# Kernel tuning notes

Measured on AMD Instinct MI355X. Metric: run time of the kernel, lower is better.

Reference implementation:

```python
import jax, jax.numpy as jnp
import numpy as np

A, C, V, G = 100000, 230, 800, 60          # athletes, countries, events, games
H, HEADS, DH = 128, 4, 32                   # hidden, gat heads, per-head dim (H = HEADS*DH)
E_AC, E_AE, E_AG, E_EG = 100000, 500000, 300000, 2000
NEG_SLOPE = 0.2


def _seg_mean(msg, idx, n):
    s = jax.ops.segment_sum(msg, idx, num_segments=n)
    cnt = jax.ops.segment_sum(jnp.ones((idx.shape[0], 1), msg.dtype), idx, num_segments=n)
    return s / jnp.maximum(cnt, 1.0)


def _sage(xs, xd, ei, Wl, bl, Wr):
    # PyG SAGEConv(mean): lin_l(mean_neighbors) + lin_r(x_dst); bias lives in lin_l
    agg = _seg_mean(xs[ei[0]], ei[1], xd.shape[0])
    return agg @ Wl + bl + xd @ Wr


def _gatv2(xs, xd, ei, Wl, bl, Wr, br, att, bias):
    # PyG GATv2Conv, concat=True, add_self_loops=False, eval mode (no dropout)
    n = xd.shape[0]
    xl = (xs @ Wl + bl).reshape(-1, HEADS, DH)   # [Ns,H,d]
    xr = (xd @ Wr + br).reshape(-1, HEADS, DH)   # [Nd,H,d]
    src, dst = ei[0], ei[1]
    e = jax.nn.leaky_relu(xl[src] + xr[dst], NEG_SLOPE)      # [E,H,d]
    logit = jnp.einsum('ehd,hd->eh', e, att)                 # [E,H]
    m = jax.ops.segment_max(logit, dst, num_segments=n)
    m = jnp.where(jnp.isneginf(m), 0.0, m)                   # empty dst segments
    ex = jnp.exp(logit - m[dst])
    den = jax.ops.segment_sum(ex, dst, num_segments=n)
    alpha = ex / (den[dst] + 1e-16)
    out = jax.ops.segment_sum(xl[src] * alpha[:, :, None], dst, num_segments=n)
    return out.reshape(n, HEADS * DH) + bias


def _mlp(x, W1, b1, W2, b2):
    return jax.nn.relu(x @ W1 + b1) @ W2 + b2


def _forward(x_athlete, x_country, x_event, x_games,
             eAW1, eAb1, eAW2, eAb2, eCW1, eCb1, eCW2, eCb2,
             eEW1, eEb1, eEW2, eEb2, eGW1, eGb1, eGW2, eGb2,
             sage_Wl, sage_bl, sage_Wr,
             gat_Wl, gat_bl, gat_Wr, gat_br, gat_att, gat_bias,
             ei_ac, ei_ae, ei_ag, ei_eg):
    x = {
        'athlete': _mlp(x_athlete, eAW1, eAb1, eAW2, eAb2),
        'country': _mlp(x_country, eCW1, eCb1, eCW2, eCb2),
        'event':   _mlp(x_event,   eEW1, eEb1, eEW2, eEb2),
        'games':   _mlp(x_games,   eGW1, eGb1, eGW2, eGb2),
    }
    rev = lambda ei: ei[::-1]
    etypes = [
        ('athlete', 'country', ei_ac), ('country', 'athlete', rev(ei_ac)),
        ('athlete', 'event',   ei_ae), ('event',   'athlete', rev(ei_ae)),
        ('athlete', 'games',   ei_ag), ('games',   'athlete', rev(ei_ag)),
        ('event',   'games',   ei_eg), ('games',   'event',   rev(ei_eg)),
    ]
    # layer 1: hetero SAGEConv, HeteroConv aggr='mean' over edge types per dst
    outs = {t: [] for t in x}
    for k, (s, d, ei) in enumerate(etypes):
        outs[d].append(_sage(x[s], x[d], ei, sage_Wl[k], sage_bl[k], sage_Wr[k]))
    x = {t: jax.nn.relu(sum(o) / len(o)) for t, o in outs.items()}
    # layer 2 (final): hetero GATv2Conv, mean over edge types per dst
    outs = {t: [] for t in x}
    for k, (s, d, ei) in enumerate(etypes):
        outs[d].append(_gatv2(x[s], x[d], ei, gat_Wl[k], gat_bl[k], gat_Wr[k],
                              gat_br[k], gat_att[k], gat_bias[k]))
    x = {t: sum(o) / len(o) for t, o in outs.items()}
    return jnp.concatenate([x['athlete'], x['country'], x['event'], x['games']], axis=0)


def setup_inputs() -> dict:
    key = jax.random.key(0)
    ks = iter(jax.random.split(key, 80))
    def nrm(shape, scale=1.0):
        return jax.random.normal(next(ks), shape, jnp.float32) * scale
    def lin(fi, fo):
        return nrm((fi, fo), 1.0 / np.sqrt(fi))
    def edges(ns, nd, E):
        s = jax.random.randint(next(ks), (E,), 0, ns)
        d = jax.random.randint(next(ks), (E,), 0, nd)
        return jnp.stack([s, d]).astype(jnp.int32)
    sc = 1.0 / np.sqrt(H)
    return {
        'x_athlete': nrm((A, 7)), 'x_country': nrm((C, 3)),
        'x_event': nrm((V, 384)), 'x_games': nrm((G, 2)),
        'ei_ac': edges(A, C, E_AC), 'ei_ae': edges(A, V, E_AE),
        'ei_ag': edges(A, G, E_AG), 'ei_eg': edges(V, G, E_EG),
        'eAW1': lin(7, H),   'eAb1': jnp.zeros((H,)), 'eAW2': lin(H, H), 'eAb2': jnp.zeros((H,)),
        'eCW1': lin(3, H),   'eCb1': jnp.zeros((H,)), 'eCW2': lin(H, H), 'eCb2': jnp.zeros((H,)),
        'eEW1': lin(384, H), 'eEb1': jnp.zeros((H,)), 'eEW2': lin(H, H), 'eEb2': jnp.zeros((H,)),
        'eGW1': lin(2, H),   'eGb1': jnp.zeros((H,)), 'eGW2': lin(H, H), 'eGb2': jnp.zeros((H,)),
        'sage_Wl': nrm((8, H, H), sc), 'sage_bl': jnp.zeros((8, H)), 'sage_Wr': nrm((8, H, H), sc),
        'gat_Wl': nrm((8, H, H), sc), 'gat_bl': jnp.zeros((8, H)),
        'gat_Wr': nrm((8, H, H), sc), 'gat_br': jnp.zeros((8, H)),
        'gat_att': nrm((8, HEADS, DH), 1.0 / np.sqrt(DH)), 'gat_bias': jnp.zeros((8, H)),
    }


def reference(x_athlete, x_country, x_event, x_games,
              eAW1, eAb1, eAW2, eAb2, eCW1, eCb1, eCW2, eCb2,
              eEW1, eEb1, eEW2, eEb2, eGW1, eGb1, eGW2, eGb2,
              sage_Wl, sage_bl, sage_Wr,
              gat_Wl, gat_bl, gat_Wr, gat_br, gat_att, gat_bias,
              ei_ac, ei_ae, ei_ag, ei_eg):
    return _forward(x_athlete, x_country, x_event, x_games,
                    eAW1, eAb1, eAW2, eAb2, eCW1, eCb1, eCW2, eCb2,
                    eEW1, eEb1, eEW2, eEb2, eGW1, eGb1, eGW2, eGb2,
                    sage_Wl, sage_bl, sage_Wr,
                    gat_Wl, gat_bl, gat_Wr, gat_br, gat_att, gat_bias,
                    ei_ac, ei_ae, ei_ag, ei_eg)
```

## Files before the change

### kernel.cpp

```cpp
#include <hip/hip_runtime.h>
#include <hip/hip_bf16.h>

#define A_N 100000
#define C_N 230
#define V_N 800
#define G_N 60

#define FLAG_RELU 2

#define SCAN_N   302080
#define SCAN_NB  295
#define E_TOTAL  1804000

#define PCHUNK 16

typedef __attribute__((ext_vector_type(8))) short short8;
typedef __attribute__((ext_vector_type(4))) float f32x4;

__device__ __forceinline__ float bf16dec(unsigned short u){
  return __uint_as_float(((unsigned)u) << 16);
}
__device__ __forceinline__ unsigned short f2b(float v){
  union { __hip_bfloat16 h; unsigned short u; } c;
  c.h = __float2bfloat16(v);
  return c.u;
}
__device__ __forceinline__ float4 ldb4(const unsigned short* p){
  uint2 v = *(const uint2*)p;
  float4 r;
  r.x = __uint_as_float(v.x << 16);
  r.y = __uint_as_float(v.x & 0xffff0000u);
  r.z = __uint_as_float(v.y << 16);
  r.w = __uint_as_float(v.y & 0xffff0000u);
  return r;
}
static inline int imin(int a, int b){ return a < b ? a : b; }

__global__ void detect_dtype(const unsigned short* __restrict__ p, int* __restrict__ flag){
  __shared__ int bad;
  if (threadIdx.x == 0) bad = 0;
  __syncthreads();
  for (int i = threadIdx.x; i < 2048; i += blockDim.x){
    float v = fabsf(bf16dec(p[i]));
    if (!(v <= 1e6f)) atomicOr(&bad, 1);
  }
  __syncthreads();
  if (threadIdx.x == 0) *flag = bad;
}

struct ConvTab { const void* src[29]; int dstoff[29]; int cum[30]; };

__global__ void convert_all(ConvTab tab, float* __restrict__ wsf,
                            const int* __restrict__ flagp, int total){
  const int f = *flagp;
  for (int idx = blockIdx.x*blockDim.x + threadIdx.x; idx < total;
       idx += gridDim.x*blockDim.x){
    int t = 0;
    while (idx >= tab.cum[t+1]) ++t;
    int l = idx - tab.cum[t];
    float v = f ? ((const float*)tab.src[t])[l]
                : bf16dec(((const unsigned short*)tab.src[t])[l]);
    wsf[tab.dstoff[t] + l] = v;
  }
}

__global__ void prep_combos(const float* __restrict__ sWr, const float* __restrict__ sbl,
                            const float* __restrict__ gbias,
                            float* __restrict__ wrcomb, float* __restrict__ sbcomb,
                            float* __restrict__ gbcomb){
  const int sets[4][3] = {{1,3,5},{0,-1,-1},{2,7,-1},{4,6,-1}};
  const float inv[4] = {1.f/3.f, 1.f, 0.5f, 0.5f};
  int idx = blockIdx.x*blockDim.x + threadIdx.x;
  if (idx >= 4*16384) return;
  int t = idx >> 14, j = idx & 16383;
  float s = 0.f;
  #pragma unroll
  for (int q = 0; q < 3; ++q){
    int k = sets[t][q];
    if (k >= 0) s += sWr[k*16384 + j];
  }
  wrcomb[idx] = s * inv[t];
  if (j < 128){
    float b1 = 0.f, b2 = 0.f;
    #pragma unroll
    for (int q = 0; q < 3; ++q){
      int k = sets[t][q];
      if (k >= 0){ b1 += sbl[k*128 + j]; b2 += gbias[k*128 + j]; }
    }
    sbcomb[t*128 + j] = b1 * inv[t];
    gbcomb[t*128 + j] = b2 * inv[t];
  }
}

__global__ void prep_bias2(const float* __restrict__ gbl, const float* __restrict__ gbr,
                           float* __restrict__ gblx, float* __restrict__ gbrx){
  int i = blockIdx.x*blockDim.x + threadIdx.x;
  if (i >= 384) return;
  const int kl[3] = {0,2,4}, kr[3] = {1,3,5};
  int rel = i >> 7, j = i & 127;
  gblx[i] = gbl[kl[rel]*128 + j];
  gbrx[i] = gbr[kr[rel]*128 + j];
}

struct SwzD { int src, dst, K, nkc, kc0, nt0; float scale; };
struct SwzTab { SwzD d[33]; int n, total; };

__global__ void swz_batch(const float* __restrict__ wsf, unsigned short* __restrict__ wsu,
                          SwzTab t){
  for (int idx = blockIdx.x*blockDim.x + threadIdx.x; idx < t.total;
       idx += gridDim.x*blockDim.x){
    int di = 0, local = idx;
    while (local >= t.d[di].K*128){ local -= t.d[di].K*128; ++di; }
    SwzD d = t.d[di];
    int j = local & 7, lane = (local>>3) & 63, rest = local >> 9;
    int kcn = d.K >> 5;
    int kc = rest % kcn, nt = rest / kcn;
    int k = kc*32 + (lane>>4)*8 + j;
    int n = nt*16 + (lane&15);
    float v = wsf[d.src + k*128 + n] * d.scale;
    wsu[(size_t)d.dst + ((size_t)((d.nt0+nt)*d.nkc + d.kc0+kc)*64 + lane)*8 + j] = f2b(v);
  }
}

__global__ void hist_plain(const int* __restrict__ dp, int E, int* __restrict__ cnt){
  int i = blockIdx.x*blockDim.x + threadIdx.x;
  if (i < E) atomicAdd(&cnt[dp[i]], 1);
}

__global__ void hist_lds(const int* __restrict__ dp, int E, int* __restrict__ cnt, int ndst){
  __shared__ int l[800];
  for (int i = threadIdx.x; i < ndst; i += blockDim.x) l[i] = 0;
  __syncthreads();
  for (int i = blockIdx.x*blockDim.x + threadIdx.x; i < E; i += gridDim.x*blockDim.x)
    atomicAdd(&l[dp[i]], 1);
  __syncthreads();
  for (int i = threadIdx.x; i < ndst; i += blockDim.x)
    if (l[i]) atomicAdd(&cnt[i], l[i]);
}

__global__ void scan1(const int* __restrict__ cnt, int* __restrict__ rp, int* __restrict__ bsum){
  __shared__ int sd[256];
  int tid = threadIdx.x, blk = blockIdx.x;
  int base = blk*1024 + tid*4;
  int4 v = *(const int4*)(cnt + base);
  int s = v.x + v.y + v.z + v.w;
  sd[tid] = s;
  __syncthreads();
  for (int off = 1; off < 256; off <<= 1){
    int t = (tid >= off) ? sd[tid-off] : 0;
    __syncthreads();
    sd[tid] += t;
    __syncthreads();
  }
  int excl = sd[tid] - s;
  rp[base+0] = excl;
  rp[base+1] = excl + v.x;
  rp[base+2] = excl + v.x + v.y;
  rp[base+3] = excl + v.x + v.y + v.z;
  if (tid == 255) bsum[blk] = sd[255];
}

__global__ void scan2(int* __restrict__ bsum){
  __shared__ int sd[512];
  int tid = threadIdx.x;
  int v = (tid < SCAN_NB) ? bsum[tid] : 0;
  sd[tid] = v;
  __syncthreads();
  for (int off = 1; off < 512; off <<= 1){
    int t = (tid >= off) ? sd[tid-off] : 0;
    __syncthreads();
    sd[tid] += t;
    __syncthreads();
  }
  if (tid < SCAN_NB) bsum[tid] = sd[tid] - v;
}

__global__ void scan3(int* __restrict__ rp, int* __restrict__ woff,
                      const int* __restrict__ bsum){
  int idx = blockIdx.x*blockDim.x + threadIdx.x;
  if (idx >= SCAN_N) return;
  int v = rp[idx] + bsum[idx >> 10];
  rp[idx] = v;
  woff[idx] = v;
}

__global__ void place_plain(const int* __restrict__ sp, const int* __restrict__ dp,
                            int E, int* __restrict__ woff, int* __restrict__ csr){
  int i = blockIdx.x*blockDim.x + threadIdx.x;
  if (i < E){
    int pos = atomicAdd(&woff[dp[i]], 1);
    csr[pos] = sp[i];
  }
}

__global__ void place_lds(const int* __restrict__ sp, const int* __restrict__ dp,
                          int E, int* __restrict__ woff, int* __restrict__ csr, int ndst){
  __shared__ int lcnt[800];
  __shared__ int lbase[800];
  const int tid = threadIdx.x;
  const int span = blockDim.x * PCHUNK;
  for (int b0 = blockIdx.x*span; b0 < E; b0 += gridDim.x*span){
    for (int i = tid; i < ndst; i += blockDim.x) lcnt[i] = 0;
    __syncthreads();
    int d[PCHUNK], s[PCHUNK], r[PCHUNK];
    #pragma unroll
    for (int j = 0; j < PCHUNK; ++j){
      int e = b0 + j*blockDim.x + tid;
      d[j] = -1;
      if (e < E){
        s[j] = sp[e];
        d[j] = dp[e];
        r[j] = atomicAdd(&lcnt[d[j]], 1);
      }
    }
    __syncthreads();
    for (int i = tid; i < ndst; i += blockDim.x){
      int c = lcnt[i];
      if (c) lbase[i] = atomicAdd(&woff[i], c);
    }
    __syncthreads();
    #pragma unroll
    for (int j = 0; j < PCHUNK; ++j)
      if (d[j] >= 0) csr[lbase[d[j]] + r[j]] = s[j];
    __syncthreads();
  }
}

__global__ void enc_l1(const float* __restrict__ X, const float* __restrict__ W1,
                       const float* __restrict__ b1, unsigned short* __restrict__ Z,
                       int M, int K){
  int idx = blockIdx.x*blockDim.x + threadIdx.x;
  if (idx >= M*128) return;
  int r = idx >> 7, c = idx & 127;
  float s = b1[c];
  for (int k = 0; k < K; ++k) s = fmaf(X[r*K + k], W1[(k<<7) + c], s);
  Z[idx] = f2b(fmaxf(s, 0.f));
}

__global__ void cvt_bf16(const float* __restrict__ src, unsigned short* __restrict__ dst, int n){
  int i = blockIdx.x*blockDim.x + threadIdx.x;
  if (i < n) dst[i] = f2b(src[i]);
}

__device__ __forceinline__ void mfma_core(
    const unsigned short* __restrict__ wsu, const float* __restrict__ wsf,
    int xoff, int xstride, int x2off, int x2stride, int kcsplit,
    int woff, int nkc, int biasoff, int yoff, int ystride,
    int M, int flags, int mblk, int nblk)
{
  int tid = threadIdx.x;
  int wv = tid >> 6, lane = tid & 63;
  int quad = lane >> 4, ml = lane & 15;
  int m0 = mblk*64 + wv*16;
  if (m0 >= M) return;
  int arow = m0 + ml;
  bool rowok = arow < M;
  f32x4 acc[8];
  #pragma unroll
  for (int i = 0; i < 8; ++i) acc[i] = (f32x4){0.f, 0.f, 0.f, 0.f};
  for (int kc = 0; kc < nkc; ++kc){
    short8 a = (short8){0,0,0,0,0,0,0,0};
    if (rowok){
      size_t ao = (kc < kcsplit)
        ? (size_t)xoff  + (size_t)arow*xstride  + kc*32 + quad*8
        : (size_t)x2off + (size_t)arow*x2stride + (kc - kcsplit)*32 + quad*8;
      a = *(const short8*)(wsu + ao);
    }
    size_t wbase = (size_t)woff + ((size_t)(nblk*8)*nkc + kc)*512 + lane*8;
    #pragma unroll
    for (int nt = 0; nt < 8; ++nt){
      short8 b = *(const short8*)(wsu + wbase + (size_t)nt*nkc*512);
      acc[nt] = __builtin_amdgcn_mfma_f32_16x16x32_bf16(a, b, acc[nt], 0, 0, 0);
    }
  }
  #pragma unroll
  for (int nt = 0; nt < 8; ++nt){
    int col = nblk*128 + nt*16 + ml;
    float bv = (biasoff >= 0) ? wsf[biasoff + col] : 0.f;
    #pragma unroll
    for (int r = 0; r < 4; ++r){
      int orow = m0 + quad*4 + r;
      if (orow < M){
        float v = acc[nt][r] + bv;
        if (flags & FLAG_RELU) v = fmaxf(v, 0.f);
        *((unsigned short*)wsu + (size_t)yoff + (size_t)orow*ystride + col) = f2b(v);
      }
    }
  }
}

__global__ __launch_bounds__(256) void mfma_gemm(
    void* ws, int xoff, int xstride, int x2off, int x2stride, int kcsplit,
    int woff, int nkc, int biasoff, int yoff, int ystride, int M, int flags)
{
  mfma_core((const unsigned short*)ws, (const float*)ws, xoff, xstride, x2off, x2stride,
            kcsplit, woff, nkc, biasoff, yoff, ystride, M, flags, blockIdx.x, blockIdx.y);
}

struct GB { int xoff, xstride, woff, biasoff, yoff, ystride, M, nkc, flags; };
struct GBTab { GB d[12]; int n; };

__global__ __launch_bounds__(256) void mfma_gemm_batch(void* ws, GBTab t){
  int di = blockIdx.x / 13, mb = blockIdx.x % 13;
  if (di >= t.n) return;
  GB g = t.d[di];
  mfma_core((const unsigned short*)ws, (const float*)ws, g.xoff, g.xstride, 0, 0, 1000,
            g.woff, g.nkc, g.biasoff, g.yoff, g.ystride, g.M, g.flags, mb, 0);
}

__global__ void sage_gather_athA(const unsigned short* __restrict__ wsu,
    const int* __restrict__ csr, const int* __restrict__ rpb,
    int uhC, int uhE, int uhG, int rp1, int rp3, int rp5, int uagg)
{
  int gid = (blockIdx.x*blockDim.x + threadIdx.x) >> 6;
  if (gid >= A_N) return;
  int lane = threadIdx.x & 63;
  int half = lane >> 5, sub = lane & 31, f = sub*4;
  int srcs[3] = {uhC, uhE, uhG};
  int sstr[3] = {256, 384, 384};
  int rps[3]  = {rp1, rp3, rp5};
  #pragma unroll
  for (int rel = 0; rel < 3; ++rel){
    const unsigned short* base = wsu + (size_t)srcs[rel] + f;
    int str = sstr[rel];
    int st = rpb[rps[rel] + gid], en = rpb[rps[rel] + gid + 1];
    float4 acc = {0.f, 0.f, 0.f, 0.f};
    int i = st + half;
    for (; i + 2 < en; i += 4){
      int s0 = csr[i], s1 = csr[i+2];
      float4 v0 = ldb4(base + (size_t)s0*str);
      float4 v1 = ldb4(base + (size_t)s1*str);
      acc.x += v0.x + v1.x; acc.y += v0.y + v1.y;
      acc.z += v0.z + v1.z; acc.w += v0.w + v1.w;
    }
    if (i < en){
      float4 v0 = ldb4(base + (size_t)csr[i]*str);
      acc.x += v0.x; acc.y += v0.y; acc.z += v0.z; acc.w += v0.w;
    }
    acc.x += __shfl_xor(acc.x, 32); acc.y += __shfl_xor(acc.y, 32);
    acc.z += __shfl_xor(acc.z, 32); acc.w += __shfl_xor(acc.w, 32);
    if (half == 0){
      int deg = en - st;
      float sc = 1.f / (float)(deg > 1 ? deg : 1);
      ushort4 o;
      o.x = f2b(acc.x*sc); o.y = f2b(acc.y*sc);
      o.z = f2b(acc.z*sc); o.w = f2b(acc.w*sc);
      *(ushort4*)((unsigned short*)wsu + (size_t)uagg + (size_t)gid*384 + rel*128 + f) = o;
    }
  }
}

struct SgD { int src, sstr, rpoff, aggoff, nd, nc; };
struct SgTab { SgD d[5]; int cumw[6]; };

__global__ void sage_gather_small(const unsigned short* __restrict__ wsu,
    float* __restrict__ wsf, const int* __restrict__ csr, const int* __restrict__ rpb,
    SgTab t)
{
  int gid = (blockIdx.x*blockDim.x + threadIdx.x) >> 6;
  if (gid >= t.cumw[5]) return;
  int di = 0;
  while (gid >= t.cumw[di+1]) ++di;
  SgD d = t.d[di];
  int local = gid - t.cumw[di];
  int row = local / d.nc, c = local - row*d.nc;
  int lane = threadIdx.x & 63;
  int half = lane >> 5, sub = lane & 31, f = sub*4;
  const unsigned short* base = wsu + (size_t)d.src + f;
  int st = rpb[d.rpoff + row], en = rpb[d.rpoff + row + 1];
  float4 acc = {0.f, 0.f, 0.f, 0.f};
  int i = st + c + half*d.nc;
  int step = 2*d.nc;
  for (; i + step < en; i += 2*step){
    int s0 = csr[i], s1 = csr[i+step];
    float4 v0 = ldb4(base + (size_t)s0*d.sstr);
    float4 v1 = ldb4(base + (size_t)s1*d.sstr);
    acc.x += v0.x + v1.x; acc.y += v0.y + v1.y;
    acc.z += v0.z + v1.z; acc.w += v0.w + v1.w;
  }
  if (i < en){
    float4 v0 = ldb4(base + (size_t)csr[i]*d.sstr);
    acc.x += v0.x; acc.y += v0.y; acc.z += v0.z; acc.w += v0.w;
  }
  acc.x += __shfl_xor(acc.x, 32); acc.y += __shfl_xor(acc.y, 32);
  acc.z += __shfl_xor(acc.z, 32); acc.w += __shfl_xor(acc.w, 32);
  if (half == 0){
    float* o = wsf + (size_t)d.aggoff + (size_t)row*128 + f;
    atomicAdd(o,   acc.x); atomicAdd(o+1, acc.y);
    atomicAdd(o+2, acc.z); atomicAdd(o+3, acc.w);
  }
}

struct AfD { int aggoff, rpoff, dstu, dstr, nd; };
struct AfTab { AfD d[5]; int n; };

__global__ void aggfin_batch(unsigned short* __restrict__ wsu, const float* __restrict__ wsf,
                             const int* __restrict__ rpb, AfTab t, int total){
  int idx = blockIdx.x*blockDim.x + threadIdx.x;
  if (idx >= total) return;
  int di = 0, local = idx;
  while (local >= t.d[di].nd*128){ local -= t.d[di].nd*128; ++di; }
  AfD d = t.d[di];
  int row = local >> 7, col = local & 127;
  int deg = rpb[d.rpoff + row + 1] - rpb[d.rpoff + row];
  float sc = 1.f / (float)(deg > 1 ? deg : 1);
  wsu[(size_t)d.dstu + (size_t)row*d.dstr + col] = f2b(wsf[(size_t)d.aggoff + local] * sc);
}

#define GAT_UPD(xv)                                                        \
  {                                                                        \
    float e0 = (xv).x + xrv.x, e1 = (xv).y + xrv.y;                        \
    float e2 = (xv).z + xrv.z, e3 = (xv).w + xrv.w;                        \
    e0 = e0 > 0.f ? e0 : 0.2f*e0; e1 = e1 > 0.f ? e1 : 0.2f*e1;            \
    e2 = e2 > 0.f ? e2 : 0.2f*e2; e3 = e3 > 0.f ? e3 : 0.2f*e3;            \
    float p = e0*av.x + e1*av.y + e2*av.z + e3*av.w;                       \
    p += __shfl_xor(p, 1); p += __shfl_xor(p, 2); p += __shfl_xor(p, 4);   \
    float nm = fmaxf(m, p);                                                \
    float scw = __expf(m - nm);                                            \
    float pe = __expf(p - nm);                                             \
    l = l*scw + pe;                                                        \
    acc.x = acc.x*scw + pe*(xv).x; acc.y = acc.y*scw + pe*(xv).y;          \
    acc.z = acc.z*scw + pe*(xv).z; acc.w = acc.w*scw + pe*(xv).w;          \
    m = nm;                                                                \
  }

#define GAT_MERGE_HALVES                                                   \
  {                                                                        \
    float mo = __shfl_xor(m, 32);                                          \
    float lo = __shfl_xor(l, 32);                                          \
    float4 ao;                                                             \
    ao.x = __shfl_xor(acc.x, 32); ao.y = __shfl_xor(acc.y, 32);            \
    ao.z = __shfl_xor(acc.z, 32); ao.w = __shfl_xor(acc.w, 32);            \
    float nm = fmaxf(m, mo);                                               \
    float w  = (m  == -INFINITY) ? 0.f : __expf(m  - nm);                  \
    float wo = (mo == -INFINITY) ? 0.f : __expf(mo - nm);                  \
    l = l*w + lo*wo;                                                       \
    acc.x = acc.x*w + ao.x*wo; acc.y = acc.y*w + ao.y*wo;                  \
    acc.z = acc.z*w + ao.z*wo; acc.w = acc.w*w + ao.w*wo;                  \
    m = nm;                                                                \
  }

__global__ void gat_ath(const unsigned short* __restrict__ wsu, const float* __restrict__ wsf,
    const int* __restrict__ csr, const int* __restrict__ rpb,
    int ugxr, int uxl1, int uxl3, int uxl5, int oatt, int rp1, int rp3, int rp5, int uout)
{
  int gid = (blockIdx.x*blockDim.x + threadIdx.x) >> 6;
  if (gid >= A_N) return;
  int lane = threadIdx.x & 63;
  int half = lane >> 5, sub = lane & 31, f = sub*4;
  int xls[3] = {uxl1, uxl3, uxl5};
  int rps[3] = {rp1, rp3, rp5};
  const int attk[3] = {1, 3, 5};
  float4 oacc = {0.f, 0.f, 0.f, 0.f};
  #pragma unroll
  for (int rel = 0; rel < 3; ++rel){
    float4 xrv = ldb4(wsu + (size_t)ugxr + (size_t)gid*384 + rel*128 + f);
    float4 av  = *(const float4*)(wsf + oatt + attk[rel]*128 + f);
    const unsigned short* base = wsu + (size_t)xls[rel] + f;
    int st = rpb[rps[rel] + gid], en = rpb[rps[rel] + gid + 1];
    float m = -INFINITY, l = 0.f;
    float4 acc = {0.f, 0.f, 0.f, 0.f};
    int i = st + half;
    for (; i + 2 < en; i += 4){
      int s0 = csr[i], s1 = csr[i+2];
      float4 x0 = ldb4(base + (size_t)s0*128);
      float4 x1 = ldb4(base + (size_t)s1*128);
      GAT_UPD(x0);
      GAT_UPD(x1);
    }
    if (i < en){
      float4 x0 = ldb4(base + (size_t)csr[i]*128);
      GAT_UPD(x0);
    }
    GAT_MERGE_HALVES;
    float inv = 1.f / (l + 1e-16f);
    oacc.x += acc.x * inv; oacc.y += acc.y * inv;
    oacc.z += acc.z * inv; oacc.w += acc.w * inv;
  }
  if (half == 0){
    ushort4 o;
    o.x = f2b(oacc.x * (1.f/3.f)); o.y = f2b(oacc.y * (1.f/3.f));
    o.z = f2b(oacc.z * (1.f/3.f)); o.w = f2b(oacc.w * (1.f/3.f));
    *(ushort4*)((unsigned short*)wsu + (size_t)uout + (size_t)gid*128 + f) = o;
  }
}

struct GoD { int xl, xlstr, xr, attoff, rpoff, prefix, nd, nc; };
struct GoTab { GoD d[5]; int cumw[6]; };

__global__ void gat_online_batch(const unsigned short* __restrict__ wsu,
    const float* __restrict__ wsf, const int* __restrict__ csr,
    const int* __restrict__ rpb, float* __restrict__ part, GoTab t)
{
  int gid = (blockIdx.x*blockDim.x + threadIdx.x) >> 6;
  if (gid >= t.cumw[5]) return;
  int di = 0;
  while (gid >= t.cumw[di+1]) ++di;
  GoD d = t.d[di];
  int local = gid - t.cumw[di];
  int row = local / d.nc, c = local - row*d.nc;
  int lane = threadIdx.x & 63;
  int half = lane >> 5, sub = lane & 31, f = sub*4, h = sub >> 3;
  float4 xrv = ldb4(wsu + (size_t)d.xr + (size_t)row*128 + f);
  float4 av  = *(const float4*)(wsf + d.attoff + f);
  const unsigned short* base = wsu + (size_t)d.xl + f;
  int st = rpb[d.rpoff + row], en = rpb[d.rpoff + row + 1];
  float m = -INFINITY, l = 0.f;
  float4 acc = {0.f, 0.f, 0.f, 0.f};
  int i = st + c + half*d.nc;
  int step = 2*d.nc;
  for (; i + step < en; i += 2*step){
    int s0 = csr[i], s1 = csr[i+step];
    float4 x0 = ldb4(base + (size_t)s0*d.xlstr);
    float4 x1 = ldb4(base + (size_t)s1*d.xlstr);
    GAT_UPD(x0);
    GAT_UPD(x1);
  }
  if (i < en){
    float4 x0 = ldb4(base + (size_t)csr[i]*d.xlstr);
    GAT_UPD(x0);
  }
  GAT_MERGE_HALVES;
  if (half == 0){
    float* pr = part + (size_t)(d.prefix + local)*136;
    if ((sub & 7) == 0){ pr[h] = m; pr[4+h] = l; }
    *(float4*)(pr + 8 + f) = acc;
  }
}

struct MgD { int prefix, outoff, nd, nc; float invS; };
struct MgTab { MgD d[5]; int cumw[6]; };

__global__ void gat_merge_batch(const float* __restrict__ part, float* __restrict__ wsf,
                                MgTab t){
  int gid = (blockIdx.x*blockDim.x + threadIdx.x) >> 6;
  if (gid >= t.cumw[5]) return;
  int di = 0;
  while (gid >= t.cumw[di+1]) ++di;
  MgD d = t.d[di];
  int row = gid - t.cumw[di];
  int lane = threadIdx.x & 63, f = lane*2, h = lane >> 4;
  float M = -INFINITY;
  for (int c = 0; c < d.nc; ++c)
    M = fmaxf(M, part[(size_t)(d.prefix + row*d.nc + c)*136 + h]);
  float L = 0.f;
  float2 acc = {0.f, 0.f};
  for (int c = 0; c < d.nc; ++c){
    const float* pr = part + (size_t)(d.prefix + row*d.nc + c)*136;
    float mc = pr[h];
    float w = (mc == -INFINITY) ? 0.f : __expf(mc - M);
    L += pr[4+h] * w;
    acc.x += pr[8+f]   * w;
    acc.y += pr[8+f+1] * w;
  }
  float inv = d.invS / (L + 1e-16f);
  float* o = wsf + (size_t)d.outoff + (size_t)row*128 + f;
  o[0] = acc.x * inv;
  o[1] = acc.y * inv;
}

__global__ void final_out(const unsigned short* __restrict__ wsu,
  const float* __restrict__ wsf, int uoutA, int oC0, int oE2, int oE7, int oG4, int oG6,
  int ogb, const int* __restrict__ flagp, void* __restrict__ dout)
{
  const int fl = *flagp;
  int idx = blockIdx.x*blockDim.x + threadIdx.x;
  const int total = 101090*128;
  if (idx >= total) return;
  int row = idx >> 7, c = idx & 127;
  float v; int t;
  if (row < A_N){ v = bf16dec(wsu[(size_t)uoutA + idx]); t = 0; }
  else if (row < A_N + C_N){ v = wsf[oC0 + (row - A_N)*128 + c]; t = 1; }
  else if (row < A_N + C_N + V_N){
    int l = (row - A_N - C_N)*128 + c;
    v = wsf[oE2 + l] + wsf[oE7 + l]; t = 2;
  } else {
    int l = (row - A_N - C_N - V_N)*128 + c;
    v = wsf[oG4 + l] + wsf[oG6 + l]; t = 3;
  }
  v += wsf[ogb + t*128 + c];
  if (fl) ((float*)dout)[idx] = v;
  else    ((__hip_bfloat16*)dout)[idx] = __float2bfloat16(v);
}

__global__ void ws_fail(float* __restrict__ out, float mb){
  if (threadIdx.x == 0 && blockIdx.x == 0) out[0] = mb;
}

extern "C" void kernel_launch(void* const* d_in, const int* in_sizes, int n_in,
                              void* d_out, int out_size, void* d_ws, size_t ws_size,
                              hipStream_t stream)
{
  float* wsf = (float*)d_ws;
  unsigned short* wsu = (unsigned short*)d_ws;
  int* flagp = (int*)d_ws;
  size_t off = 16;
  auto alloc = [&](size_t n){ size_t o = off; off += (n + 15) & ~(size_t)15; return (int)o; };
  auto allocU = [&](size_t nu){ return 2*alloc((nu + 1)/2); };

  static const int conv_in_idx[29] = {0,1,2,3, 8,9,10,11, 12,13,14,15, 16,17,18,19,
                                      20,21,22,23, 24,25,26, 27,28,29,30,31,32};
  static const int conv_n[29] = {700000,690,307200,120,
                                 896,128,16384,128, 384,128,16384,128,
                                 49152,128,16384,128, 256,128,16384,128,
                                 131072,1024,131072, 131072,1024,131072,1024,1024,1024};
  ConvTab tab;
  int coff[29];
  int total = 0;
  for (int i = 0; i < 29; ++i){
    tab.src[i] = d_in[conv_in_idx[i]];
    coff[i] = alloc((size_t)conv_n[i]);
    tab.dstoff[i] = coff[i];
    tab.cum[i] = total; total += conv_n[i];
  }
  tab.cum[29] = total;

  const int o_sWl = coff[20], o_sbl = coff[21];
  const int o_gWl = coff[23], o_gbl = coff[24], o_gWr = coff[25], o_gbr = coff[26];
  const int o_gatt = coff[27], o_gbias = coff[28];

  int o_wrcomb = alloc(4*16384);
  int o_sbcomb = alloc(512);
  int o_gbcomb = alloc(512);
  int o_gblx = alloc(384);
  int o_gbrx = alloc(384);
  int o_cnt  = alloc(SCAN_N);
  int o_rp   = alloc(SCAN_N);
  int o_woff = alloc(SCAN_N);
  int o_bsum = alloc(1024);
  int o_csr  = alloc(E_TOTAL);
  int o_part = alloc((size_t)22320*136);
  int o_aggS = alloc((size_t)1950*128);
  int o_outC0 = alloc(230*128);
  int o_outE2 = alloc(800*128);
  int o_outE7 = alloc(800*128);
  int o_outG4 = alloc(60*128);
  int o_outG6 = alloc(60*128);

  int u_bswz = allocU(573440);
  int u_xEb  = allocU(307200);
  int u_zC   = allocU(230*128);
  int u_zE   = allocU(800*128);
  int u_zG   = allocU(60*128);
  int u_sxC  = allocU(230*256);
  int u_sxE  = allocU(800*384);
  int u_sxG  = allocU(60*384);
  int u_yC   = allocU(230*128);
  int u_yE   = allocU(800*128);
  int u_yG   = allocU(60*128);
  int u_xl1  = allocU(230*128);
  int u_xl3  = allocU(800*128);
  int u_xl5  = allocU(60*128);
  int u_xl6  = allocU(800*128);
  int u_xl7  = allocU(60*128);
  int u_xr0  = allocU(230*128);
  int u_xr2  = allocU(800*128);
  int u_xr4  = allocU(60*128);
  int u_xr6  = allocU(60*128);
  int u_xr7  = allocU(800*128);
  int u_big0 = allocU((size_t)A_N*128);
  int u_bigH = allocU((size_t)A_N*128);
  int u_bigA = allocU((size_t)A_N*384);

  if (off*4 > ws_size){
    ws_fail<<<1, 64, 0, stream>>>((float*)d_out, (float)((off*4) >> 20));
    return;
  }

  const int u_eAW2 = u_bswz + 0,      u_eCW2 = u_bswz + 16384;
  const int u_eEW2 = u_bswz + 32768,  u_eGW2 = u_bswz + 49152;
  const int u_eEW1 = u_bswz + 65536;
  const int u_sxAW = u_bswz + 114688, u_sxCW = u_bswz + 180224;
  const int u_sxEW = u_bswz + 212992, u_sxGW = u_bswz + 262144;
  const int u_gxlW = u_bswz + 311296, u_gxrW = u_bswz + 360448;
  int u_smW[10];
  for (int i = 0; i < 10; ++i) u_smW[i] = u_bswz + 409600 + i*16384;

  const int n_nodes[4] = {A_N, C_N, V_N, G_N};
  const int et_dst[8] = {1,0,2,0,3,0,3,2};
  const int et_ei[8]  = {4,4,5,5,6,6,7,7};
  const int et_rev[8] = {0,1,0,1,0,1,0,1};
  const int et_E[8]   = {100000,100000,500000,500000,300000,300000,2000,2000};

  const int* esp[8]; const int* edp[8]; int rowbase[8];
  {
    int rb = 0;
    for (int k = 0; k < 8; ++k){
      const int* ei = (const int*)d_in[et_ei[k]];
      int E = et_E[k];
      esp[k] = ei + (et_rev[k] ? E : 0);
      edp[k] = ei + (et_rev[k] ? 0 : E);
      rowbase[k] = rb; rb += n_nodes[et_dst[k]];
    }
  }
  int* rpb_p  = (int*)(wsf + o_rp);
  int* csr_p  = (int*)(wsf + o_csr);

  detect_dtype<<<1, 256, 0, stream>>>((const unsigned short*)d_in[2], flagp);
  convert_all<<<2048, 256, 0, stream>>>(tab, wsf, flagp, total);
  prep_combos<<<(4*16384 + 255)/256, 256, 0, stream>>>(wsf + coff[22], wsf + o_sbl,
      wsf + o_gbias, wsf + o_wrcomb, wsf + o_sbcomb, wsf + o_gbcomb);
  prep_bias2<<<2, 256, 0, stream>>>(wsf + o_gbl, wsf + o_gbr, wsf + o_gblx, wsf + o_gbrx);

  SwzTab st; int sn = 0, stotal = 0;
  auto push = [&](int src, int K, int dst, int nkc, int kc0, int nt0, float sc){
    st.d[sn++] = SwzD{src, dst, K, nkc, kc0, nt0, sc};
    stotal += K*128;
  };
  push(coff[6],  128, u_eAW2, 4, 0, 0, 1.f);
  push(coff[10], 128, u_eCW2, 4, 0, 0, 1.f);
  push(coff[14], 128, u_eEW2, 4, 0, 0, 1.f);
  push(coff[18], 128, u_eGW2, 4, 0, 0, 1.f);
  push(coff[12], 384, u_eEW1, 12, 0, 0, 1.f);
  push(o_wrcomb + 0,     128, u_sxAW, 16, 0,  0, 1.f);
  push(o_sWl + 1*16384,  128, u_sxAW, 16, 4,  0, 1.f/3.f);
  push(o_sWl + 3*16384,  128, u_sxAW, 16, 8,  0, 1.f/3.f);
  push(o_sWl + 5*16384,  128, u_sxAW, 16, 12, 0, 1.f/3.f);
  push(o_wrcomb + 16384, 128, u_sxCW, 8, 0, 0, 1.f);
  push(o_sWl + 0*16384,  128, u_sxCW, 8, 4, 0, 1.f);
  push(o_wrcomb + 32768, 128, u_sxEW, 12, 0, 0, 1.f);
  push(o_sWl + 2*16384,  128, u_sxEW, 12, 4, 0, 0.5f);
  push(o_sWl + 7*16384,  128, u_sxEW, 12, 8, 0, 0.5f);
  push(o_wrcomb + 49152, 128, u_sxGW, 12, 0, 0, 1.f);
  push(o_sWl + 4*16384,  128, u_sxGW, 12, 4, 0, 0.5f);
  push(o_sWl + 6*16384,  128, u_sxGW, 12, 8, 0, 0.5f);
  push(o_gWl + 0*16384, 128, u_gxlW, 4, 0, 0,  1.f);
  push(o_gWl + 2*16384, 128, u_gxlW, 4, 0, 8,  1.f);
  push(o_gWl + 4*16384, 128, u_gxlW, 4, 0, 16, 1.f);
  push(o_gWr + 1*16384, 128, u_gxrW, 4, 0, 0,  1.f);
  push(o_gWr + 3*16384, 128, u_gxrW, 4, 0, 8,  1.f);
  push(o_gWr + 5*16384, 128, u_gxrW, 4, 0, 16, 1.f);
  const int xlk[5] = {1,3,5,6,7};
  for (int i = 0; i < 5; ++i) push(o_gWl + xlk[i]*16384, 128, u_smW[i], 4, 0, 0, 1.f);
  const int xrk[5] = {0,2,4,6,7};
  for (int i = 0; i < 5; ++i) push(o_gWr + xrk[i]*16384, 128, u_smW[5+i], 4, 0, 0, 1.f);
  st.n = sn; st.total = stotal;
  swz_batch<<<(stotal + 255)/256, 256, 0, stream>>>(wsf, wsu, st);

  hipMemsetAsync(wsf + o_cnt, 0, (size_t)SCAN_N*4, stream);
  for (int k = 0; k < 8; ++k){
    int E = et_E[k], nd = n_nodes[et_dst[k]];
    if (nd <= 800)
      hist_lds<<<imin(256, (E + 255)/256), 256, 0, stream>>>(edp[k], E,
          (int*)(wsf + o_cnt) + rowbase[k], nd);
    else
      hist_plain<<<(E + 255)/256, 256, 0, stream>>>(edp[k], E,
          (int*)(wsf + o_cnt) + rowbase[k]);
  }
  scan1<<<SCAN_NB, 256, 0, stream>>>((int*)(wsf + o_cnt), rpb_p, (int*)(wsf + o_bsum));
  scan2<<<1, 512, 0, stream>>>((int*)(wsf + o_bsum));
  scan3<<<(SCAN_N + 255)/256, 256, 0, stream>>>(rpb_p, (int*)(wsf + o_woff),
                                                (int*)(wsf + o_bsum));
  for (int k = 0; k < 8; ++k){
    int E = et_E[k], nd = n_nodes[et_dst[k]];
    if (nd <= 800){
      int span = 256*PCHUNK;
      place_lds<<<imin(304, (E + span - 1)/span), 256, 0, stream>>>(
          esp[k], edp[k], E, (int*)(wsf + o_woff) + rowbase[k], csr_p, nd);
    } else {
      place_plain<<<(E + 255)/256, 256, 0, stream>>>(esp[k], edp[k], E,
          (int*)(wsf + o_woff) + rowbase[k], csr_p);
    }
  }

  enc_l1<<<(A_N*128 + 255)/256, 256, 0, stream>>>(wsf + coff[0], wsf + coff[4],
      wsf + coff[5], wsu + u_big0, A_N, 7);
  enc_l1<<<(C_N*128 + 255)/256, 256, 0, stream>>>(wsf + coff[1], wsf + coff[8],
      wsf + coff[9], wsu + u_zC, C_N, 3);
  enc_l1<<<(G_N*128 + 255)/256, 256, 0, stream>>>(wsf + coff[3], wsf + coff[16],
      wsf + coff[17], wsu + u_zG, G_N, 2);
  cvt_bf16<<<(307200 + 255)/256, 256, 0, stream>>>(wsf + coff[2], wsu + u_xEb, 307200);

  GBTab e1; e1.n = 3;
  e1.d[0] = GB{u_zC, 128, u_eCW2, coff[11], u_sxC, 256, C_N, 4, 0};
  e1.d[1] = GB{u_xEb, 384, u_eEW1, coff[13], u_zE, 128, V_N, 12, FLAG_RELU};
  e1.d[2] = GB{u_zG, 128, u_eGW2, coff[19], u_sxG, 384, G_N, 4, 0};
  mfma_gemm_batch<<<3*13, 256, 0, stream>>>(d_ws, e1);
  GBTab e2; e2.n = 1;
  e2.d[0] = GB{u_zE, 128, u_eEW2, coff[15], u_sxE, 384, V_N, 4, 0};
  mfma_gemm_batch<<<13, 256, 0, stream>>>(d_ws, e2);
  mfma_gemm<<<dim3((A_N + 63)/64, 1), 256, 0, stream>>>(d_ws, u_big0, 128, 0, 0, 1000,
      u_eAW2, 4, coff[7], u_bigH, 128, A_N, 0);

  sage_gather_athA<<<(A_N*64 + 255)/256, 256, 0, stream>>>(wsu, csr_p, rpb_p,
      u_sxC, u_sxE, u_sxG, rowbase[1], rowbase[3], rowbase[5], u_bigA);
  hipMemsetAsync(wsf + o_aggS, 0, (size_t)1950*128*4, stream);
  const int b0 = o_aggS, b2 = o_aggS + 230*128, b7 = b2 + 800*128,
            b4 = b7 + 800*128, b6 = b4 + 60*128;
  SgTab sg;
  sg.d[0] = SgD{u_bigH, 128, rowbase[0], b0, C_N, 8};
  sg.d[1] = SgD{u_bigH, 128, rowbase[2], b2, V_N, 8};
  sg.d[2] = SgD{u_sxG, 384, rowbase[7], b7, V_N, 8};
  sg.d[3] = SgD{u_bigH, 128, rowbase[4], b4, G_N, 64};
  sg.d[4] = SgD{u_sxE, 384, rowbase[6], b6, G_N, 64};
  sg.cumw[0] = 0;
  {
    int c = 0;
    for (int i = 0; i < 5; ++i){ c += sg.d[i].nd*sg.d[i].nc; sg.cumw[i+1] = c; }
  }
  sage_gather_small<<<(sg.cumw[5]*64 + 255)/256, 256, 0, stream>>>(wsu, wsf, csr_p, rpb_p, sg);
  AfTab af; af.n = 5;
  af.d[0] = AfD{b0, rowbase[0], u_sxC + 128, 256, C_N};
  af.d[1] = AfD{b2, rowbase[2], u_sxE + 128, 384, V_N};
  af.d[2] = AfD{b7, rowbase[7], u_sxE + 256, 384, V_N};
  af.d[3] = AfD{b4, rowbase[4], u_sxG + 128, 384, G_N};
  af.d[4] = AfD{b6, rowbase[6], u_sxG + 256, 384, G_N};
  int aftot = 1950*128;
  aggfin_batch<<<(aftot + 255)/256, 256, 0, stream>>>(wsu, wsf, rpb_p, af, aftot);
  GBTab sgm; sgm.n = 3;
  sgm.d[0] = GB{u_sxC, 256, u_sxCW, o_sbcomb + 128, u_yC, 128, C_N, 8,  FLAG_RELU};
  sgm.d[1] = GB{u_sxE, 384, u_sxEW, o_sbcomb + 256, u_yE, 128, V_N, 12, FLAG_RELU};
  sgm.d[2] = GB{u_sxG, 384, u_sxGW, o_sbcomb + 384, u_yG, 128, G_N, 12, FLAG_RELU};
  mfma_gemm_batch<<<3*13, 256, 0, stream>>>(d_ws, sgm);
  mfma_gemm<<<dim3((A_N + 63)/64, 1), 256, 0, stream>>>(d_ws, u_bigH, 128, u_bigA, 384, 4,
      u_sxAW, 16, o_sbcomb, u_big0, 128, A_N, FLAG_RELU);

  mfma_gemm<<<dim3((A_N + 63)/64, 3), 256, 0, stream>>>(d_ws, u_big0, 128, 0, 0, 1000,
      u_gxlW, 4, o_gblx, u_bigA, 384, A_N, 0);
  GBTab gm; gm.n = 10;
  gm.d[0] = GB{u_yC, 128, u_smW[0], o_gbl + 1*128, u_xl1, 128, C_N, 4, 0};
  gm.d[1] = GB{u_yE, 128, u_smW[1], o_gbl + 3*128, u_xl3, 128, V_N, 4, 0};
  gm.d[2] = GB{u_yG, 128, u_smW[2], o_gbl + 5*128, u_xl5, 128, G_N, 4, 0};
  gm.d[3] = GB{u_yE, 128, u_smW[3], o_gbl + 6*128, u_xl6, 128, V_N, 4, 0};
  gm.d[4] = GB{u_yG, 128, u_smW[4], o_gbl + 7*128, u_xl7, 128, G_N, 4, 0};
  gm.d[5] = GB{u_yC, 128, u_smW[5], o_gbr + 0*128, u_xr0, 128, C_N, 4, 0};
  gm.d[6] = GB{u_yE, 128, u_smW[6], o_gbr + 2*128, u_xr2, 128, V_N, 4, 0};
  gm.d[7] = GB{u_yG, 128, u_smW[7], o_gbr + 4*128, u_xr4, 128, G_N, 4, 0};
  gm.d[8] = GB{u_yG, 128, u_smW[8], o_gbr + 6*128, u_xr6, 128, G_N, 4, 0};
  gm.d[9] = GB{u_yE, 128, u_smW[9], o_gbr + 7*128, u_xr7, 128, V_N, 4, 0};
  mfma_gemm_batch<<<10*13, 256, 0, stream>>>(d_ws, gm);

  GoTab go;
  go.d[0] = GoD{u_bigA + 0,   384, u_xr0, o_gatt + 0*128, rowbase[0], 0,     C_N, 8};
  go.d[1] = GoD{u_bigA + 128, 384, u_xr2, o_gatt + 2*128, rowbase[2], 1840,  V_N, 8};
  go.d[2] = GoD{u_bigA + 256, 384, u_xr4, o_gatt + 4*128, rowbase[4], 8240,  G_N, 64};
  go.d[3] = GoD{u_xl6, 128,        u_xr6, o_gatt + 6*128, rowbase[6], 12080, G_N, 64};
  go.d[4] = GoD{u_xl7, 128,        u_xr7, o_gatt + 7*128, rowbase[7], 15920, V_N, 8};
  go.cumw[0] = 0;
  {
    int c = 0;
    for (int i = 0; i < 5; ++i){ c += go.d[i].nd*go.d[i].nc; go.cumw[i+1] = c; }
  }
  gat_online_batch<<<(go.cumw[5]*64 + 255)/256, 256, 0, stream>>>(wsu, wsf, csr_p, rpb_p,
      wsf + o_part, go);

  mfma_gemm<<<dim3((A_N + 63)/64, 3), 256, 0, stream>>>(d_ws, u_big0, 128, 0, 0, 1000,
      u_gxrW, 4, o_gbrx, u_bigA, 384, A_N, 0);
  gat_ath<<<(A_N*64 + 255)/256, 256, 0, stream>>>(wsu, wsf, csr_p, rpb_p,
      u_bigA, u_xl1, u_xl3, u_xl5, o_gatt, rowbase[1], rowbase[3], rowbase[5], u_bigH);

  MgTab mg;
  mg.d[0] = MgD{0,     o_outC0, C_N, 8,  1.0f};
  mg.d[1] = MgD{1840,  o_outE2, V_N, 8,  0.5f};
  mg.d[2] = MgD{8240,  o_outG4, G_N, 64, 0.5f};
  mg.d[3] = MgD{12080, o_outG6, G_N, 64, 0.5f};
  mg.d[4] = MgD{15920, o_outE7, V_N, 8,  0.5f};
  mg.cumw[0] = 0;
  {
    int c = 0;
    for (int i = 0; i < 5; ++i){ c += mg.d[i].nd; mg.cumw[i+1] = c; }
  }
  gat_merge_batch<<<(mg.cumw[5]*64 + 255)/256, 256, 0, stream>>>(wsf + o_part, wsf, mg);

  final_out<<<(101090*128 + 255)/256, 256, 0, stream>>>(wsu, wsf, u_bigH,
      o_outC0, o_outE2, o_outE7, o_outG4, o_outG6, o_gbcomb, flagp, d_out);
}
```

Before: 1.093 ms.

## Batch histogram, placement, encoder, gemm and gather launches into fewer kernels

Merges many small kernel launches into table-driven batched kernels: per-relation histogram and CSR placement, the encoder first layers plus bf16 conversion, several GEMM groups, and the athlete and small-node SAGE gathers. It also raises the per-row split counts for the small-node gathers and GAT partials, and adds a paired online-softmax update. The aim is to cut launch overhead and tail idleness from underfilled small grids. In exchange it adds block-to-task lookup loops and possibly uneven work within a merged grid.

```diff
diff --git a/kernel.cpp b/kernel.cpp
--- a/kernel.cpp
+++ b/kernel.cpp
@@ -66,8 +66,10 @@
 
 __global__ void prep_combos(const float* __restrict__ sWr, const float* __restrict__ sbl,
                             const float* __restrict__ gbias,
+                            const float* __restrict__ gbl, const float* __restrict__ gbr,
                             float* __restrict__ wrcomb, float* __restrict__ sbcomb,
-                            float* __restrict__ gbcomb){
+                            float* __restrict__ gbcomb,
+                            float* __restrict__ gblx, float* __restrict__ gbrx){
   const int sets[4][3] = {{1,3,5},{0,-1,-1},{2,7,-1},{4,6,-1}};
   const float inv[4] = {1.f/3.f, 1.f, 0.5f, 0.5f};
   int idx = blockIdx.x*blockDim.x + threadIdx.x;
@@ -90,16 +92,12 @@
     sbcomb[t*128 + j] = b1 * inv[t];
     gbcomb[t*128 + j] = b2 * inv[t];
   }
-}
-
-__global__ void prep_bias2(const float* __restrict__ gbl, const float* __restrict__ gbr,
-                           float* __restrict__ gblx, float* __restrict__ gbrx){
-  int i = blockIdx.x*blockDim.x + threadIdx.x;
-  if (i >= 384) return;
-  const int kl[3] = {0,2,4}, kr[3] = {1,3,5};
-  int rel = i >> 7, j = i & 127;
-  gblx[i] = gbl[kl[rel]*128 + j];
-  gbrx[i] = gbr[kr[rel]*128 + j];
+  if (idx < 384){
+    const int kl[3] = {0,2,4}, kr[3] = {1,3,5};
+    int rel = idx >> 7, jj = idx & 127;
+    gblx[idx] = gbl[kl[rel]*128 + jj];
+    gbrx[idx] = gbr[kr[rel]*128 + jj];
+  }
 }
 
 struct SwzD { int src, dst, K, nkc, kc0, nt0; float scale; };
@@ -122,20 +120,84 @@
   }
 }
 
-__global__ void hist_plain(const int* __restrict__ dp, int E, int* __restrict__ cnt){
-  int i = blockIdx.x*blockDim.x + threadIdx.x;
-  if (i < E) atomicAdd(&cnt[dp[i]], 1);
-}
-
-__global__ void hist_lds(const int* __restrict__ dp, int E, int* __restrict__ cnt, int ndst){
+struct HTab {
+  const int* dp[8];
+  int E[8], cntoff[8], ndst[8], mode[8], bstart[9];
+};
+
+__global__ void hist_all(HTab t, int* __restrict__ cnt){
   __shared__ int l[800];
-  for (int i = threadIdx.x; i < ndst; i += blockDim.x) l[i] = 0;
-  __syncthreads();
-  for (int i = blockIdx.x*blockDim.x + threadIdx.x; i < E; i += gridDim.x*blockDim.x)
-    atomicAdd(&l[dp[i]], 1);
-  __syncthreads();
-  for (int i = threadIdx.x; i < ndst; i += blockDim.x)
-    if (l[i]) atomicAdd(&cnt[i], l[i]);
+  int k = 0;
+  while ((int)blockIdx.x >= t.bstart[k+1]) ++k;
+  int lb = blockIdx.x - t.bstart[k], nb = t.bstart[k+1] - t.bstart[k];
+  const int* dp = t.dp[k];
+  int E = t.E[k];
+  int* c = cnt + t.cntoff[k];
+  if (t.mode[k]){
+    int nd = t.ndst[k];
+    for (int i = threadIdx.x; i < nd; i += blockDim.x) l[i] = 0;
+    __syncthreads();
+    for (int i = lb*blockDim.x + threadIdx.x; i < E; i += nb*blockDim.x)
+      atomicAdd(&l[dp[i]], 1);
+    __syncthreads();
+    for (int i = threadIdx.x; i < nd; i += blockDim.x)
+      if (l[i]) atomicAdd(&c[i], l[i]);
+  } else {
+    for (int i = lb*blockDim.x + threadIdx.x; i < E; i += nb*blockDim.x)
+      atomicAdd(&c[dp[i]], 1);
+  }
+}
+
+struct PTab {
+  const int* sp[8]; const int* dp[8];
+  int E[8], woffoff[8], ndst[8], mode[8], bstart[9];
+};
+
+__global__ void place_all(PTab t, int* __restrict__ woffb, int* __restrict__ csr){
+  __shared__ int lcnt[800];
+  __shared__ int lbase[800];
+  int k = 0;
+  while ((int)blockIdx.x >= t.bstart[k+1]) ++k;
+  int lb = blockIdx.x - t.bstart[k], nb = t.bstart[k+1] - t.bstart[k];
+  const int* sp = t.sp[k];
+  const int* dp = t.dp[k];
+  int E = t.E[k];
+  int* woff = woffb + t.woffoff[k];
+  const int tid = threadIdx.x;
+  if (t.mode[k]){
+    int nd = t.ndst[k];
+    const int span = blockDim.x * PCHUNK;
+    for (int b0 = lb*span; b0 < E; b0 += nb*span){
+      for (int i = tid; i < nd; i += blockDim.x) lcnt[i] = 0;
+      __syncthreads();
+      int d[PCHUNK], s[PCHUNK], r[PCHUNK];
+      #pragma unroll
+      for (int j = 0; j < PCHUNK; ++j){
+        int e = b0 + j*blockDim.x + tid;
+        d[j] = -1;
+        if (e < E){
+          s[j] = sp[e];
+          d[j] = dp[e];
+          r[j] = atomicAdd(&lcnt[d[j]], 1);
+        }
+      }
+      __syncthreads();
+      for (int i = tid; i < nd; i += blockDim.x){
+        int c = lcnt[i];
+        if (c) lbase[i] = atomicAdd(&woff[i], c);
+      }
+      __syncthreads();
+      #pragma unroll
+      for (int j = 0; j < PCHUNK; ++j)
+        if (d[j] >= 0) csr[lbase[d[j]] + r[j]] = s[j];
+      __syncthreads();
+    }
+  } else {
+    for (int i = lb*blockDim.x + tid; i < E; i += nb*blockDim.x){
+      int pos = atomicAdd(&woff[dp[i]], 1);
+      csr[pos] = sp[i];
+    }
+  }
 }
 
 __global__ void scan1(const int* __restrict__ cnt, int* __restrict__ rp, int* __restrict__ bsum){
@@ -184,62 +246,29 @@
   woff[idx] = v;
 }
 
-__global__ void place_plain(const int* __restrict__ sp, const int* __restrict__ dp,
-                            int E, int* __restrict__ woff, int* __restrict__ csr){
-  int i = blockIdx.x*blockDim.x + threadIdx.x;
-  if (i < E){
-    int pos = atomicAdd(&woff[dp[i]], 1);
-    csr[pos] = sp[i];
-  }
-}
-
-__global__ void place_lds(const int* __restrict__ sp, const int* __restrict__ dp,
-                          int E, int* __restrict__ woff, int* __restrict__ csr, int ndst){
-  __shared__ int lcnt[800];
-  __shared__ int lbase[800];
-  const int tid = threadIdx.x;
-  const int span = blockDim.x * PCHUNK;
-  for (int b0 = blockIdx.x*span; b0 < E; b0 += gridDim.x*span){
-    for (int i = tid; i < ndst; i += blockDim.x) lcnt[i] = 0;
-    __syncthreads();
-    int d[PCHUNK], s[PCHUNK], r[PCHUNK];
-    #pragma unroll
-    for (int j = 0; j < PCHUNK; ++j){
-      int e = b0 + j*blockDim.x + tid;
-      d[j] = -1;
-      if (e < E){
-        s[j] = sp[e];
-        d[j] = dp[e];
-        r[j] = atomicAdd(&lcnt[d[j]], 1);
-      }
-    }
-    __syncthreads();
-    for (int i = tid; i < ndst; i += blockDim.x){
-      int c = lcnt[i];
-      if (c) lbase[i] = atomicAdd(&woff[i], c);
-    }
-    __syncthreads();
-    #pragma unroll
-    for (int j = 0; j < PCHUNK; ++j)
-      if (d[j] >= 0) csr[lbase[d[j]] + r[j]] = s[j];
-    __syncthreads();
-  }
-}
-
-__global__ void enc_l1(const float* __restrict__ X, const float* __restrict__ W1,
-                       const float* __restrict__ b1, unsigned short* __restrict__ Z,
-                       int M, int K){
-  int idx = blockIdx.x*blockDim.x + threadIdx.x;
-  if (idx >= M*128) return;
-  int r = idx >> 7, c = idx & 127;
-  float s = b1[c];
-  for (int k = 0; k < K; ++k) s = fmaf(X[r*K + k], W1[(k<<7) + c], s);
-  Z[idx] = f2b(fmaxf(s, 0.f));
-}
-
-__global__ void cvt_bf16(const float* __restrict__ src, unsigned short* __restrict__ dst, int n){
-  int i = blockIdx.x*blockDim.x + threadIdx.x;
-  if (i < n) dst[i] = f2b(src[i]);
+struct EncTab {
+  int cum[5];
+  int xoff[4], woff[4], boff[4], zoff[4], K[4];
+};
+
+__global__ void enc_batch(const float* __restrict__ wsf, unsigned short* __restrict__ wsu,
+                          EncTab t){
+  for (int idx = blockIdx.x*blockDim.x + threadIdx.x; idx < t.cum[4];
+       idx += gridDim.x*blockDim.x){
+    int s = 0;
+    while (idx >= t.cum[s+1]) ++s;
+    int local = idx - t.cum[s];
+    if (s < 3){
+      int r = local >> 7, c = local & 127;
+      int K = t.K[s];
+      float acc = wsf[t.boff[s] + c];
+      for (int k = 0; k < K; ++k)
+        acc = fmaf(wsf[t.xoff[s] + r*K + k], wsf[t.woff[s] + (k<<7) + c], acc);
+      wsu[(size_t)t.zoff[s] + (size_t)r*128 + c] = f2b(fmaxf(acc, 0.f));
+    } else {
+      wsu[(size_t)t.zoff[3] + local] = f2b(wsf[t.xoff[3] + local]);
+    }
+  }
 }
 
 __device__ __forceinline__ void mfma_core(
@@ -289,105 +318,93 @@
   }
 }
 
-__global__ __launch_bounds__(256) void mfma_gemm(
-    void* ws, int xoff, int xstride, int x2off, int x2stride, int kcsplit,
-    int woff, int nkc, int biasoff, int yoff, int ystride, int M, int flags)
-{
-  mfma_core((const unsigned short*)ws, (const float*)ws, xoff, xstride, x2off, x2stride,
-            kcsplit, woff, nkc, biasoff, yoff, ystride, M, flags, blockIdx.x, blockIdx.y);
-}
-
-struct GB { int xoff, xstride, woff, biasoff, yoff, ystride, M, nkc, flags; };
-struct GBTab { GB d[12]; int n; };
-
-__global__ __launch_bounds__(256) void mfma_gemm_batch(void* ws, GBTab t){
-  int di = blockIdx.x / 13, mb = blockIdx.x % 13;
-  if (di >= t.n) return;
-  GB g = t.d[di];
-  mfma_core((const unsigned short*)ws, (const float*)ws, g.xoff, g.xstride, 0, 0, 1000,
-            g.woff, g.nkc, g.biasoff, g.yoff, g.ystride, g.M, g.flags, mb, 0);
-}
-
-__global__ void sage_gather_athA(const unsigned short* __restrict__ wsu,
-    const int* __restrict__ csr, const int* __restrict__ rpb,
+struct GB2 { int xoff, xstride, x2off, x2stride, kcsplit, woff, nkc, biasoff,
+             yoff, ystride, M, flags, nblk; };
+struct GB2Tab { GB2 d[13]; int b0[14]; int n; };
+
+__global__ __launch_bounds__(256) void mfma_gemm_b2(void* ws, GB2Tab t){
+  int b = blockIdx.x, di = 0;
+  while (b >= t.b0[di+1]) ++di;
+  GB2 g = t.d[di];
+  mfma_core((const unsigned short*)ws, (const float*)ws, g.xoff, g.xstride,
+            g.x2off, g.x2stride, g.kcsplit, g.woff, g.nkc, g.biasoff,
+            g.yoff, g.ystride, g.M, g.flags, b - t.b0[di], g.nblk);
+}
+
+struct SgD { int src, sstr, rpoff, aggoff, nd, nc; };
+struct SgTab { SgD d[5]; int cumw[6]; };
+
+__global__ void sage_all(const unsigned short* __restrict__ wsu, float* __restrict__ wsf,
+    const int* __restrict__ csr, const int* __restrict__ rpb, SgTab t,
     int uhC, int uhE, int uhG, int rp1, int rp3, int rp5, int uagg)
 {
   int gid = (blockIdx.x*blockDim.x + threadIdx.x) >> 6;
-  if (gid >= A_N) return;
   int lane = threadIdx.x & 63;
   int half = lane >> 5, sub = lane & 31, f = sub*4;
-  int srcs[3] = {uhC, uhE, uhG};
-  int sstr[3] = {256, 384, 384};
-  int rps[3]  = {rp1, rp3, rp5};
-  #pragma unroll
-  for (int rel = 0; rel < 3; ++rel){
-    const unsigned short* base = wsu + (size_t)srcs[rel] + f;
-    int str = sstr[rel];
-    int st = rpb[rps[rel] + gid], en = rpb[rps[rel] + gid + 1];
+  if (gid < A_N){
+    int srcs[3] = {uhC, uhE, uhG};
+    int sstr[3] = {256, 384, 384};
+    int rps[3]  = {rp1, rp3, rp5};
+    #pragma unroll
+    for (int rel = 0; rel < 3; ++rel){
+      const unsigned short* base = wsu + (size_t)srcs[rel] + f;
+      int str = sstr[rel];
+      int st = rpb[rps[rel] + gid], en = rpb[rps[rel] + gid + 1];
+      float4 acc = {0.f, 0.f, 0.f, 0.f};
+      int i = st + half;
+      for (; i + 2 < en; i += 4){
+        int s0 = csr[i], s1 = csr[i+2];
+        float4 v0 = ldb4(base + (size_t)s0*str);
+        float4 v1 = ldb4(base + (size_t)s1*str);
+        acc.x += v0.x + v1.x; acc.y += v0.y + v1.y;
+        acc.z += v0.z + v1.z; acc.w += v0.w + v1.w;
+      }
+      if (i < en){
+        float4 v0 = ldb4(base + (size_t)csr[i]*str);
+        acc.x += v0.x; acc.y += v0.y; acc.z += v0.z; acc.w += v0.w;
+      }
+      acc.x += __shfl_xor(acc.x, 32); acc.y += __shfl_xor(acc.y, 32);
+      acc.z += __shfl_xor(acc.z, 32); acc.w += __shfl_xor(acc.w, 32);
+      if (half == 0){
+        int deg = en - st;
+        float sc = 1.f / (float)(deg > 1 ? deg : 1);
+        ushort4 o;
+        o.x = f2b(acc.x*sc); o.y = f2b(acc.y*sc);
+        o.z = f2b(acc.z*sc); o.w = f2b(acc.w*sc);
+        *(ushort4*)((unsigned short*)wsu + (size_t)uagg + (size_t)gid*384 + rel*128 + f) = o;
+      }
+    }
+  } else {
+    int wid = gid - A_N;
+    if (wid >= t.cumw[5]) return;
+    int di = 0;
+    while (wid >= t.cumw[di+1]) ++di;
+    SgD d = t.d[di];
+    int local = wid - t.cumw[di];
+    int row = local / d.nc, c = local - row*d.nc;
+    const unsigned short* base = wsu + (size_t)d.src + f;
+    int st = rpb[d.rpoff + row], en = rpb[d.rpoff + row + 1];
     float4 acc = {0.f, 0.f, 0.f, 0.f};
-    int i = st + half;
-    for (; i + 2 < en; i += 4){
-      int s0 = csr[i], s1 = csr[i+2];
-      float4 v0 = ldb4(base + (size_t)s0*str);
-      float4 v1 = ldb4(base + (size_t)s1*str);
+    int i = st + c + half*d.nc;
+    int step = 2*d.nc;
+    for (; i + step < en; i += 2*step){
+      int s0 = csr[i], s1 = csr[i+step];
+      float4 v0 = ldb4(base + (size_t)s0*d.sstr);
+      float4 v1 = ldb4(base + (size_t)s1*d.sstr);
       acc.x += v0.x + v1.x; acc.y += v0.y + v1.y;
       acc.z += v0.z + v1.z; acc.w += v0.w + v1.w;
     }
     if (i < en){
-      float4 v0 = ldb4(base + (size_t)csr[i]*str);
+      float4 v0 = ldb4(base + (size_t)csr[i]*d.sstr);
       acc.x += v0.x; acc.y += v0.y; acc.z += v0.z; acc.w += v0.w;
     }
     acc.x += __shfl_xor(acc.x, 32); acc.y += __shfl_xor(acc.y, 32);
     acc.z += __shfl_xor(acc.z, 32); acc.w += __shfl_xor(acc.w, 32);
     if (half == 0){
-      int deg = en - st;
-      float sc = 1.f / (float)(deg > 1 ? deg : 1);
-      ushort4 o;
-      o.x = f2b(acc.x*sc); o.y = f2b(acc.y*sc);
-      o.z = f2b(acc.z*sc); o.w = f2b(acc.w*sc);
-      *(ushort4*)((unsigned short*)wsu + (size_t)uagg + (size_t)gid*384 + rel*128 + f) = o;
-    }
-  }
-}
-
-struct SgD { int src, sstr, rpoff, aggoff, nd, nc; };
-struct SgTab { SgD d[5]; int cumw[6]; };
-
-__global__ void sage_gather_small(const unsigned short* __restrict__ wsu,
-    float* __restrict__ wsf, const int* __restrict__ csr, const int* __restrict__ rpb,
-    SgTab t)
-{
-  int gid = (blockIdx.x*blockDim.x + threadIdx.x) >> 6;
-  if (gid >= t.cumw[5]) return;
-  int di = 0;
-  while (gid >= t.cumw[di+1]) ++di;
-  SgD d = t.d[di];
-  int local = gid - t.cumw[di];
-  int row = local / d.nc, c = local - row*d.nc;
-  int lane = threadIdx.x & 63;
-  int half = lane >> 5, sub = lane & 31, f = sub*4;
-  const unsigned short* base = wsu + (size_t)d.src + f;
-  int st = rpb[d.rpoff + row], en = rpb[d.rpoff + row + 1];
-  float4 acc = {0.f, 0.f, 0.f, 0.f};
-  int i = st + c + half*d.nc;
-  int step = 2*d.nc;
-  for (; i + step < en; i += 2*step){
-    int s0 = csr[i], s1 = csr[i+step];
-    float4 v0 = ldb4(base + (size_t)s0*d.sstr);
-    float4 v1 = ldb4(base + (size_t)s1*d.sstr);
-    acc.x += v0.x + v1.x; acc.y += v0.y + v1.y;
-    acc.z += v0.z + v1.z; acc.w += v0.w + v1.w;
-  }
-  if (i < en){
-    float4 v0 = ldb4(base + (size_t)csr[i]*d.sstr);
-    acc.x += v0.x; acc.y += v0.y; acc.z += v0.z; acc.w += v0.w;
-  }
-  acc.x += __shfl_xor(acc.x, 32); acc.y += __shfl_xor(acc.y, 32);
-  acc.z += __shfl_xor(acc.z, 32); acc.w += __shfl_xor(acc.w, 32);
-  if (half == 0){
-    float* o = wsf + (size_t)d.aggoff + (size_t)row*128 + f;
-    atomicAdd(o,   acc.x); atomicAdd(o+1, acc.y);
-    atomicAdd(o+2, acc.z); atomicAdd(o+3, acc.w);
+      float* o = wsf + (size_t)d.aggoff + (size_t)row*128 + f;
+      atomicAdd(o,   acc.x); atomicAdd(o+1, acc.y);
+      atomicAdd(o+2, acc.z); atomicAdd(o+3, acc.w);
+    }
   }
 }
 
@@ -407,20 +424,44 @@
   wsu[(size_t)d.dstu + (size_t)row*d.dstr + col] = f2b(wsf[(size_t)d.aggoff + local] * sc);
 }
 
-#define GAT_UPD(xv)                                                        \
+#define GAT_LOGIT(xv, pout)                                                \
   {                                                                        \
     float e0 = (xv).x + xrv.x, e1 = (xv).y + xrv.y;                        \
     float e2 = (xv).z + xrv.z, e3 = (xv).w + xrv.w;                        \
     e0 = e0 > 0.f ? e0 : 0.2f*e0; e1 = e1 > 0.f ? e1 : 0.2f*e1;            \
     e2 = e2 > 0.f ? e2 : 0.2f*e2; e3 = e3 > 0.f ? e3 : 0.2f*e3;            \
-    float p = e0*av.x + e1*av.y + e2*av.z + e3*av.w;                       \
-    p += __shfl_xor(p, 1); p += __shfl_xor(p, 2); p += __shfl_xor(p, 4);   \
+    pout = e0*av.x + e1*av.y + e2*av.z + e3*av.w;                          \
+    pout += __shfl_xor(pout, 1); pout += __shfl_xor(pout, 2);              \
+    pout += __shfl_xor(pout, 4);                                           \
+  }
+
+#define GAT_UPD(xv)                                                        \
+  {                                                                        \
+    float p;                                                               \
+    GAT_LOGIT(xv, p);                                                      \
     float nm = fmaxf(m, p);                                                \
     float scw = __expf(m - nm);                                            \
     float pe = __expf(p - nm);                                             \
     l = l*scw + pe;                                                        \
     acc.x = acc.x*scw + pe*(xv).x; acc.y = acc.y*scw + pe*(xv).y;          \
     acc.z = acc.z*scw + pe*(xv).z; acc.w = acc.w*scw + pe*(xv).w;          \
+    m = nm;                                                                \
+  }
+
+#define GAT_UPD2(x0, x1)                                                   \
+  {                                                                        \
+    float p0, p1;                                                          \
+    GAT_LOGIT(x0, p0);                                                     \
+    GAT_LOGIT(x1, p1);                                                     \
+    float nm = fmaxf(m, fmaxf(p0, p1));                                    \
+    float scw = __expf(m - nm);                                            \
+    float pe0 = __expf(p0 - nm);                                           \
+    float pe1 = __expf(p1 - nm);                                           \
+    l = l*scw + pe0 + pe1;                                                 \
+    acc.x = acc.x*scw + pe0*(x0).x + pe1*(x1).x;                           \
+    acc.y = acc.y*scw + pe0*(x0).y + pe1*(x1).y;                           \
+    acc.z = acc.z*scw + pe0*(x0).z + pe1*(x1).z;                           \
+    acc.w = acc.w*scw + pe0*(x0).w + pe1*(x1).w;                           \
     m = nm;                                                                \
   }
 
@@ -465,8 +506,7 @@
       int s0 = csr[i], s1 = csr[i+2];
       float4 x0 = ldb4(base + (size_t)s0*128);
       float4 x1 = ldb4(base + (size_t)s1*128);
-      GAT_UPD(x0);
-      GAT_UPD(x1);
+      GAT_UPD2(x0, x1);
     }
     if (i < en){
       float4 x0 = ldb4(base + (size_t)csr[i]*128);
@@ -513,8 +553,7 @@
     int s0 = csr[i], s1 = csr[i+step];
     float4 x0 = ldb4(base + (size_t)s0*d.xlstr);
     float4 x1 = ldb4(base + (size_t)s1*d.xlstr);
-    GAT_UPD(x0);
-    GAT_UPD(x1);
+    GAT_UPD2(x0, x1);
   }
   if (i < en){
     float4 x0 = ldb4(base + (size_t)csr[i]*d.xlstr);
@@ -629,7 +668,7 @@
   int o_woff = alloc(SCAN_N);
   int o_bsum = alloc(1024);
   int o_csr  = alloc(E_TOTAL);
-  int o_part = alloc((size_t)22320*136);
+  int o_part = alloc((size_t)36160*136);
   int o_aggS = alloc((size_t)1950*128);
   int o_outC0 = alloc(230*128);
   int o_outE2 = alloc(800*128);
@@ -699,8 +738,8 @@
   detect_dtype<<<1, 256, 0, stream>>>((const unsigned short*)d_in[2], flagp);
   convert_all<<<2048, 256, 0, stream>>>(tab, wsf, flagp, total);
   prep_combos<<<(4*16384 + 255)/256, 256, 0, stream>>>(wsf + coff[22], wsf + o_sbl,
-      wsf + o_gbias, wsf + o_wrcomb, wsf + o_sbcomb, wsf + o_gbcomb);
-  prep_bias2<<<2, 256, 0, stream>>>(wsf + o_gbl, wsf + o_gbr, wsf + o_gblx, wsf + o_gbrx);
+      wsf + o_gbias, wsf + o_gbl, wsf + o_gbr,
+      wsf + o_wrcomb, wsf + o_sbcomb, wsf + o_gbcomb, wsf + o_gblx, wsf + o_gbrx);
 
   SwzTab st; int sn = 0, stotal = 0;
   auto push = [&](int src, int K, int dst, int nkc, int kc0, int nt0, float sc){
@@ -738,67 +777,87 @@
   swz_batch<<<(stotal + 255)/256, 256, 0, stream>>>(wsf, wsu, st);
 
   hipMemsetAsync(wsf + o_cnt, 0, (size_t)SCAN_N*4, stream);
-  for (int k = 0; k < 8; ++k){
-    int E = et_E[k], nd = n_nodes[et_dst[k]];
-    if (nd <= 800)
-      hist_lds<<<imin(256, (E + 255)/256), 256, 0, stream>>>(edp[k], E,
-          (int*)(wsf + o_cnt) + rowbase[k], nd);
-    else
-      hist_plain<<<(E + 255)/256, 256, 0, stream>>>(edp[k], E,
-          (int*)(wsf + o_cnt) + rowbase[k]);
-  }
-  scan1<<<SCAN_NB, 256, 0, stream>>>((int*)(wsf + o_cnt), rpb_p, (int*)(wsf + o_bsum));
-  scan2<<<1, 512, 0, stream>>>((int*)(wsf + o_bsum));
-  scan3<<<(SCAN_N + 255)/256, 256, 0, stream>>>(rpb_p, (int*)(wsf + o_woff),
-                                                (int*)(wsf + o_bsum));
-  for (int k = 0; k < 8; ++k){
-    int E = et_E[k], nd = n_nodes[et_dst[k]];
-    if (nd <= 800){
-      int span = 256*PCHUNK;
-      place_lds<<<imin(304, (E + span - 1)/span), 256, 0, stream>>>(
-          esp[k], edp[k], E, (int*)(wsf + o_woff) + rowbase[k], csr_p, nd);
-    } else {
-      place_plain<<<(E + 255)/256, 256, 0, stream>>>(esp[k], edp[k], E,
-          (int*)(wsf + o_woff) + rowbase[k], csr_p);
-    }
-  }
-
-  enc_l1<<<(A_N*128 + 255)/256, 256, 0, stream>>>(wsf + coff[0], wsf + coff[4],
-      wsf + coff[5], wsu + u_big0, A_N, 7);
-  enc_l1<<<(C_N*128 + 255)/256, 256, 0, stream>>>(wsf + coff[1], wsf + coff[8],
-      wsf + coff[9], wsu + u_zC, C_N, 3);
-  enc_l1<<<(G_N*128 + 255)/256, 256, 0, stream>>>(wsf + coff[3], wsf + coff[16],
-      wsf + coff[17], wsu + u_zG, G_N, 2);
-  cvt_bf16<<<(307200 + 255)/256, 256, 0, stream>>>(wsf + coff[2], wsu + u_xEb, 307200);
-
-  GBTab e1; e1.n = 3;
-  e1.d[0] = GB{u_zC, 128, u_eCW2, coff[11], u_sxC, 256, C_N, 4, 0};
-  e1.d[1] = GB{u_xEb, 384, u_eEW1, coff[13], u_zE, 128, V_N, 12, FLAG_RELU};
-  e1.d[2] = GB{u_zG, 128, u_eGW2, coff[19], u_sxG, 384, G_N, 4, 0};
-  mfma_gemm_batch<<<3*13, 256, 0, stream>>>(d_ws, e1);
-  GBTab e2; e2.n = 1;
-  e2.d[0] = GB{u_zE, 128, u_eEW2, coff[15], u_sxE, 384, V_N, 4, 0};
-  mfma_gemm_batch<<<13, 256, 0, stream>>>(d_ws, e2);
-  mfma_gemm<<<dim3((A_N + 63)/64, 1), 256, 0, stream>>>(d_ws, u_big0, 128, 0, 0, 1000,
-      u_eAW2, 4, coff[7], u_bigH, 128, A_N, 0);
-
-  sage_gather_athA<<<(A_N*64 + 255)/256, 256, 0, stream>>>(wsu, csr_p, rpb_p,
-      u_sxC, u_sxE, u_sxG, rowbase[1], rowbase[3], rowbase[5], u_bigA);
+  {
+    HTab ht; PTab pt;
+    int hb = 0, pb = 0;
+    for (int k = 0; k < 8; ++k){
+      int E = et_E[k], nd = n_nodes[et_dst[k]];
+      int small = (nd <= 800);
+      ht.dp[k] = edp[k]; ht.E[k] = E; ht.cntoff[k] = rowbase[k];
+      ht.ndst[k] = nd; ht.mode[k] = small;
+      ht.bstart[k] = hb;
+      hb += small ? imin(128, (E + 255)/256) : (E + 255)/256;
+      pt.sp[k] = esp[k]; pt.dp[k] = edp[k]; pt.E[k] = E;
+      pt.woffoff[k] = rowbase[k]; pt.ndst[k] = nd; pt.mode[k] = small;
+      pt.bstart[k] = pb;
+      pb += small ? imin(128, (E + 256*PCHUNK - 1)/(256*PCHUNK)) : (E + 255)/256;
+    }
+    ht.bstart[8] = hb; pt.bstart[8] = pb;
+    hist_all<<<hb, 256, 0, stream>>>(ht, (int*)(wsf + o_cnt));
+    scan1<<<SCAN_NB, 256, 0, stream>>>((int*)(wsf + o_cnt), rpb_p, (int*)(wsf + o_bsum));
+    scan2<<<1, 512, 0, stream>>>((int*)(wsf + o_bsum));
+    scan3<<<(SCAN_N + 255)/256, 256, 0, stream>>>(rpb_p, (int*)(wsf + o_woff),
+                                                  (int*)(wsf + o_bsum));
+    place_all<<<pb, 256, 0, stream>>>(pt, (int*)(wsf + o_woff), csr_p);
+  }
+
+  {
+    EncTab et2;
+    et2.cum[0] = 0;
+    et2.cum[1] = A_N*128;
+    et2.cum[2] = et2.cum[1] + C_N*128;
+    et2.cum[3] = et2.cum[2] + G_N*128;
+    et2.cum[4] = et2.cum[3] + 307200;
+    et2.xoff[0] = coff[0]; et2.woff[0] = coff[4];  et2.boff[0] = coff[5];
+    et2.zoff[0] = u_big0;  et2.K[0] = 7;
+    et2.xoff[1] = coff[1]; et2.woff[1] = coff[8];  et2.boff[1] = coff[9];
+    et2.zoff[1] = u_zC;    et2.K[1] = 3;
+    et2.xoff[2] = coff[3]; et2.woff[2] = coff[16]; et2.boff[2] = coff[17];
+    et2.zoff[2] = u_zG;    et2.K[2] = 2;
+    et2.xoff[3] = coff[2]; et2.woff[3] = 0; et2.boff[3] = 0;
+    et2.zoff[3] = u_xEb;   et2.K[3] = 0;
+    enc_batch<<<(et2.cum[4] + 255)/256, 256, 0, stream>>>(wsf, wsu, et2);
+  }
+
+  auto pushG = [&](GB2Tab& T, GB2 g){
+    T.d[T.n] = g;
+    T.b0[T.n + 1] = T.b0[T.n] + (g.M + 63)/64;
+    T.n++;
+  };
+
+  {
+    GB2Tab t; t.n = 0; t.b0[0] = 0;
+    pushG(t, GB2{u_zC, 128, 0,0,1000, u_eCW2, 4, coff[11], u_sxC, 256, C_N, 0, 0});
+    pushG(t, GB2{u_xEb, 384, 0,0,1000, u_eEW1, 12, coff[13], u_zE, 128, V_N, FLAG_RELU, 0});
+    pushG(t, GB2{u_zG, 128, 0,0,1000, u_eGW2, 4, coff[19], u_sxG, 384, G_N, 0, 0});
+    pushG(t, GB2{u_big0, 128, 0,0,1000, u_eAW2, 4, coff[7], u_bigH, 128, A_N, 0, 0});
+    mfma_gemm_b2<<<t.b0[t.n], 256, 0, stream>>>(d_ws, t);
+  }
+  {
+    GB2Tab t; t.n = 0; t.b0[0] = 0;
+    pushG(t, GB2{u_zE, 128, 0,0,1000, u_eEW2, 4, coff[15], u_sxE, 384, V_N, 0, 0});
+    mfma_gemm_b2<<<t.b0[t.n], 256, 0, stream>>>(d_ws, t);
+  }
+
   hipMemsetAsync(wsf + o_aggS, 0, (size_t)1950*128*4, stream);
   const int b0 = o_aggS, b2 = o_aggS + 230*128, b7 = b2 + 800*128,
             b4 = b7 + 800*128, b6 = b4 + 60*128;
   SgTab sg;
-  sg.d[0] = SgD{u_bigH, 128, rowbase[0], b0, C_N, 8};
-  sg.d[1] = SgD{u_bigH, 128, rowbase[2], b2, V_N, 8};
+  sg.d[0] = SgD{u_bigH, 128, rowbase[0], b0, C_N, 32};
+  sg.d[1] = SgD{u_bigH, 128, rowbase[2], b2, V_N, 16};
   sg.d[2] = SgD{u_sxG, 384, rowbase[7], b7, V_N, 8};
-  sg.d[3] = SgD{u_bigH, 128, rowbase[4], b4, G_N, 64};
-  sg.d[4] = SgD{u_sxE, 384, rowbase[6], b6, G_N, 64};
+  sg.d[3] = SgD{u_bigH, 128, rowbase[4], b4, G_N, 128};
+  sg.d[4] = SgD{u_sxE, 384, rowbase[6], b6, G_N, 32};
   sg.cumw[0] = 0;
   {
     int c = 0;
     for (int i = 0; i < 5; ++i){ c += sg.d[i].nd*sg.d[i].nc; sg.cumw[i+1] = c; }
   }
-  sage_gather_small<<<(sg.cumw[5]*64 + 255)/256, 256, 0, stream>>>(wsu, wsf, csr_p, rpb_p, sg);
+  {
+    int waves = A_N + sg.cumw[5];
+    sage_all<<<(waves*64 + 255)/256, 256, 0, stream>>>(wsu, wsf, csr_p, rpb_p, sg,
+        u_sxC, u_sxE, u_sxG, rowbase[1], rowbase[3], rowbase[5], u_bigA);
+  }
   AfTab af; af.n = 5;
   af.d[0] = AfD{b0, rowbase[0], u_sxC + 128, 256, C_N};
   af.d[1] = AfD{b2, rowbase[2], u_sxE + 128, 384, V_N};
@@ -807,35 +866,40 @@
   af.d[4] = AfD{b6, rowbase[6], u_sxG + 256, 384, G_N};
   int aftot = 1950*128;
   aggfin_batch<<<(aftot + 255)/256, 256, 0, stream>>>(wsu, wsf, rpb_p, af, aftot);
-  GBTab sgm; sgm.n = 3;
-  sgm.d[0] = GB{u_sxC, 256, u_sxCW, o_sbcomb + 128, u_yC, 128, C_N, 8,  FLAG_RELU};
-  sgm.d[1] = GB{u_sxE, 384, u_sxEW, o_sbcomb + 256, u_yE, 128, V_N, 12, FLAG_RELU};
-  sgm.d[2] = GB{u_sxG, 384, u_sxGW, o_sbcomb + 384, u_yG, 128, G_N, 12, FLAG_RELU};
-  mfma_gemm_batch<<<3*13, 256, 0, stream>>>(d_ws, sgm);
-  mfma_gemm<<<dim3((A_N + 63)/64, 1), 256, 0, stream>>>(d_ws, u_bigH, 128, u_bigA, 384, 4,
-      u_sxAW, 16, o_sbcomb, u_big0, 128, A_N, FLAG_RELU);
-
-  mfma_gemm<<<dim3((A_N + 63)/64, 3), 256, 0, stream>>>(d_ws, u_big0, 128, 0, 0, 1000,
-      u_gxlW, 4, o_gblx, u_bigA, 384, A_N, 0);
-  GBTab gm; gm.n = 10;
-  gm.d[0] = GB{u_yC, 128, u_smW[0], o_gbl + 1*128, u_xl1, 128, C_N, 4, 0};
-  gm.d[1] = GB{u_yE, 128, u_smW[1], o_gbl + 3*128, u_xl3, 128, V_N, 4, 0};
-  gm.d[2] = GB{u_yG, 128, u_smW[2], o_gbl + 5*128, u_xl5, 128, G_N, 4, 0};
-  gm.d[3] = GB{u_yE, 128, u_smW[3], o_gbl + 6*128, u_xl6, 128, V_N, 4, 0};
-  gm.d[4] = GB{u_yG, 128, u_smW[4], o_gbl + 7*128, u_xl7, 128, G_N, 4, 0};
-  gm.d[5] = GB{u_yC, 128, u_smW[5], o_gbr + 0*128, u_xr0, 128, C_N, 4, 0};
-  gm.d[6] = GB{u_yE, 128, u_smW[6], o_gbr + 2*128, u_xr2, 128, V_N, 4, 0};
-  gm.d[7] = GB{u_yG, 128, u_smW[7], o_gbr + 4*128, u_xr4, 128, G_N, 4, 0};
-  gm.d[8] = GB{u_yG, 128, u_smW[8], o_gbr + 6*128, u_xr6, 128, G_N, 4, 0};
-  gm.d[9] = GB{u_yE, 128, u_smW[9], o_gbr + 7*128, u_xr7, 128, V_N, 4, 0};
-  mfma_gemm_batch<<<10*13, 256, 0, stream>>>(d_ws, gm);
+
+  {
+    GB2Tab t; t.n = 0; t.b0[0] = 0;
+    pushG(t, GB2{u_sxC, 256, 0,0,1000, u_sxCW, 8,  o_sbcomb + 128, u_yC, 128, C_N, FLAG_RELU, 0});
+    pushG(t, GB2{u_sxE, 384, 0,0,1000, u_sxEW, 12, o_sbcomb + 256, u_yE, 128, V_N, FLAG_RELU, 0});
+    pushG(t, GB2{u_sxG, 384, 0,0,1000, u_sxGW, 12, o_sbcomb + 384, u_yG, 128, G_N, FLAG_RELU, 0});
+    pushG(t, GB2{u_bigH, 128, u_bigA, 384, 4, u_sxAW, 16, o_sbcomb, u_big0, 128, A_N, FLAG_RELU, 0});
+    mfma_gemm_b2<<<t.b0[t.n], 256, 0, stream>>>(d_ws, t);
+  }
+
+  {
+    GB2Tab t; t.n = 0; t.b0[0] = 0;
+    pushG(t, GB2{u_big0, 128, 0,0,1000, u_gxlW, 4, o_gblx, u_bigA, 384, A_N, 0, 0});
+    pushG(t, GB2{u_big0, 128, 0,0,1000, u_gxlW, 4, o_gblx, u_bigA, 384, A_N, 0, 1});
+    pushG(t, GB2{u_big0, 128, 0,0,1000, u_gxlW, 4, o_gblx, u_bigA, 384, A_N, 0, 2});
+    pushG(t, GB2{u_yC, 128, 0,0,1000, u_smW[0], 4, o_gbl + 1*128, u_xl1, 128, C_N, 0, 0});
+    pushG(t, GB2{u_yE, 128, 0,0,1000, u_smW[1], 4, o_gbl + 3*128, u_xl3, 128, V_N, 0, 0});
+    pushG(t, GB2{u_yG, 128, 0,0,1000, u_smW[2], 4, o_gbl + 5*128, u_xl5, 128, G_N, 0, 0});
+    pushG(t, GB2{u_yE, 128, 0,0,1000, u_smW[3], 4, o_gbl + 6*128, u_xl6, 128, V_N, 0, 0});
+    pushG(t, GB2{u_yG, 128, 0,0,1000, u_smW[4], 4, o_gbl + 7*128, u_xl7, 128, G_N, 0, 0});
+    pushG(t, GB2{u_yC, 128, 0,0,1000, u_smW[5], 4, o_gbr + 0*128, u_xr0, 128, C_N, 0, 0});
+    pushG(t, GB2{u_yE, 128, 0,0,1000, u_smW[6], 4, o_gbr + 2*128, u_xr2, 128, V_N, 0, 0});
+    pushG(t, GB2{u_yG, 128, 0,0,1000, u_smW[7], 4, o_gbr + 4*128, u_xr4, 128, G_N, 0, 0});
+    pushG(t, GB2{u_yG, 128, 0,0,1000, u_smW[8], 4, o_gbr + 6*128, u_xr6, 128, G_N, 0, 0});
+    pushG(t, GB2{u_yE, 128, 0,0,1000, u_smW[9], 4, o_gbr + 7*128, u_xr7, 128, V_N, 0, 0});
+    mfma_gemm_b2<<<t.b0[t.n], 256, 0, stream>>>(d_ws, t);
+  }
 
   GoTab go;
-  go.d[0] = GoD{u_bigA + 0,   384, u_xr0, o_gatt + 0*128, rowbase[0], 0,     C_N, 8};
-  go.d[1] = GoD{u_bigA + 128, 384, u_xr2, o_gatt + 2*128, rowbase[2], 1840,  V_N, 8};
-  go.d[2] = GoD{u_bigA + 256, 384, u_xr4, o_gatt + 4*128, rowbase[4], 8240,  G_N, 64};
-  go.d[3] = GoD{u_xl6, 128,        u_xr6, o_gatt + 6*128, rowbase[6], 12080, G_N, 64};
-  go.d[4] = GoD{u_xl7, 128,        u_xr7, o_gatt + 7*128, rowbase[7], 15920, V_N, 8};
+  go.d[0] = GoD{u_bigA + 0,   384, u_xr0, o_gatt + 0*128, rowbase[0], 0,     C_N, 32};
+  go.d[1] = GoD{u_bigA + 128, 384, u_xr2, o_gatt + 2*128, rowbase[2], 7360,  V_N, 16};
+  go.d[2] = GoD{u_bigA + 256, 384, u_xr4, o_gatt + 4*128, rowbase[4], 20160, G_N, 128};
+  go.d[3] = GoD{u_xl6, 128,        u_xr6, o_gatt + 6*128, rowbase[6], 27840, G_N, 32};
+  go.d[4] = GoD{u_xl7, 128,        u_xr7, o_gatt + 7*128, rowbase[7], 29760, V_N, 8};
   go.cumw[0] = 0;
   {
     int c = 0;
@@ -844,17 +908,22 @@
   gat_online_batch<<<(go.cumw[5]*64 + 255)/256, 256, 0, stream>>>(wsu, wsf, csr_p, rpb_p,
       wsf + o_part, go);
 
-  mfma_gemm<<<dim3((A_N + 63)/64, 3), 256, 0, stream>>>(d_ws, u_big0, 128, 0, 0, 1000,
-      u_gxrW, 4, o_gbrx, u_bigA, 384, A_N, 0);
+  {
+    GB2Tab t; t.n = 0; t.b0[0] = 0;
+    pushG(t, GB2{u_big0, 128, 0,0,1000, u_gxrW, 4, o_gbrx, u_bigA, 384, A_N, 0, 0});
+    pushG(t, GB2{u_big0, 128, 0,0,1000, u_gxrW, 4, o_gbrx, u_bigA, 384, A_N, 0, 1});
+    pushG(t, GB2{u_big0, 128, 0,0,1000, u_gxrW, 4, o_gbrx, u_bigA, 384, A_N, 0, 2});
+    mfma_gemm_b2<<<t.b0[t.n], 256, 0, stream>>>(d_ws, t);
+  }
   gat_ath<<<(A_N*64 + 255)/256, 256, 0, stream>>>(wsu, wsf, csr_p, rpb_p,
       u_bigA, u_xl1, u_xl3, u_xl5, o_gatt, rowbase[1], rowbase[3], rowbase[5], u_bigH);
 
   MgTab mg;
-  mg.d[0] = MgD{0,     o_outC0, C_N, 8,  1.0f};
-  mg.d[1] = MgD{1840,  o_outE2, V_N, 8,  0.5f};
-  mg.d[2] = MgD{8240,  o_outG4, G_N, 64, 0.5f};
-  mg.d[3] = MgD{12080, o_outG6, G_N, 64, 0.5f};
-  mg.d[4] = MgD{15920, o_outE7, V_N, 8,  0.5f};
+  mg.d[0] = MgD{0,     o_outC0, C_N, 32,  1.0f};
+  mg.d[1] = MgD{7360,  o_outE2, V_N, 16,  0.5f};
+  mg.d[2] = MgD{20160, o_outG4, G_N, 128, 0.5f};
+  mg.d[3] = MgD{27840, o_outG6, G_N, 32,  0.5f};
+  mg.d[4] = MgD{29760, o_outE7, V_N, 8,   0.5f};
   mg.cumw[0] = 0;
   {
     int c = 0;
```

After: 1.021 ms. 6.6% less time.
